# Performance work log

Measured on AMD Instinct MI355X. Metric: run time of the kernel, lower is better.

## Reference

```python
import jax, jax.numpy as jnp
import numpy as np

NUM_HEADS, NUM_KV, HEAD_DIM, WIDTH = 4, 1, 256, 1024
MASK_FILL = -2.3819763e38


def _apply_rope(x, positions, max_wavelength=10000.0):
    # x: [B, T, N, H], positions: [B, T]
    d = x.shape[-1]
    freq_exp = (2.0 / d) * jnp.arange(d // 2, dtype=jnp.float32)
    timescale = max_wavelength ** freq_exp                      # [H/2]
    radians = positions[..., None].astype(jnp.float32) / timescale  # [B, T, H/2]
    radians = radians[..., None, :]                             # [B, T, 1, H/2]
    sin, cos = jnp.sin(radians), jnp.cos(radians)
    x1, x2 = jnp.split(x, 2, axis=-1)
    out = jnp.concatenate([x1 * cos - x2 * sin, x2 * cos + x1 * sin], axis=-1)
    return out.astype(x.dtype)


def _rmsnorm(x, scale):
    var = jnp.mean(jnp.square(x.astype(jnp.float32)), axis=-1, keepdims=True)
    normed = x * jax.lax.rsqrt(var + 1e-6)
    return (normed * (1 + scale)).astype(x.dtype)


def setup_inputs() -> dict:
    key = jax.random.key(0)
    ks = jax.random.split(key, 7)
    B, T, S = 8, 512, 2048
    return {
        "x": jax.random.normal(ks[0], (B, T, WIDTH), jnp.float32),
        "mem_seq": jax.random.normal(ks[1], (B, S, WIDTH), jnp.float32),
        "mem_mask": jax.random.randint(ks[2], (B, S), 0, 2).astype(bool),
        "rms_scale": jax.random.normal(ks[3], (WIDTH,), jnp.float32) * 0.02,
        "q_w": jax.random.normal(ks[4], (NUM_HEADS, WIDTH, HEAD_DIM), jnp.float32) / np.sqrt(WIDTH),
        "kv_w": jax.random.normal(ks[5], (2, NUM_KV, WIDTH, HEAD_DIM), jnp.float32) / np.sqrt(WIDTH),
        "out_w": jax.random.normal(ks[6], (NUM_HEADS, HEAD_DIM, WIDTH), jnp.float32) / np.sqrt(NUM_HEADS * HEAD_DIM),
    }


def reference(x, mem_seq, mem_mask, rms_scale, q_w, kv_w, out_w):
    B, S, _ = mem_seq.shape
    T = x.shape[1]
    G = NUM_HEADS // NUM_KV  # query heads per kv head

    xn = _rmsnorm(x, rms_scale)          # shared RMSNorm params
    mn = _rmsnorm(mem_seq, rms_scale)

    q = jnp.einsum("BTD,NDH->BTNH", xn, q_w)          # [B,T,4,256]
    kv = jnp.einsum("BSD,cKDH->cBSKH", mn, kv_w)      # [2,B,S,1,256]
    k, v = kv[0], kv[1]

    q_pos = jnp.broadcast_to(jnp.arange(S, T + S), (B, T))
    k_pos = jnp.broadcast_to(jnp.arange(S), (B, S))
    q = _apply_rope(q, q_pos) * (HEAD_DIM ** -0.5)
    k = _apply_rope(k, k_pos)

    q = q.reshape(B, T, NUM_KV, G, HEAD_DIM)
    logits = jnp.einsum("BTKGH,BSKH->BKGTS", q, k, preferred_element_type=jnp.float32)
    masked = jnp.where(mem_mask[:, None, None, None, :], logits, MASK_FILL)
    probs = jax.nn.softmax(masked, axis=-1).astype(x.dtype)
    enc = jnp.einsum("BKGTS,BSKH->BTKGH", probs, v).reshape(B, T, NUM_HEADS, HEAD_DIM)
    return jnp.einsum("BTNH,NHD->BTD", enc, out_w)
```

## Files before the change

kernel.cpp:

```cpp
#include <hip/hip_runtime.h>
#include <stdint.h>

typedef __bf16   bf16x8 __attribute__((ext_vector_type(8)));
typedef float    f32x4  __attribute__((ext_vector_type(4)));
typedef float    f32x16 __attribute__((ext_vector_type(16)));
typedef uint16_t u16x8  __attribute__((ext_vector_type(8)));
typedef uint16_t u16x4  __attribute__((ext_vector_type(4)));
typedef uint32_t u32x4  __attribute__((ext_vector_type(4)));

#define DEVFN static __device__ __forceinline__

DEVFN uint16_t f2bf(float f){
  uint32_t u = __builtin_bit_cast(uint32_t, f);
  u += 0x7fffu + ((u >> 16) & 1u);
  return (uint16_t)(u >> 16);
}
DEVFN float bf2f(uint16_t h){
  return __builtin_bit_cast(float, (uint32_t)h << 16);
}
DEVFN bf16x8 ldbf8(const uint16_t* p){
  return __builtin_bit_cast(bf16x8, *(const u16x8*)p);
}
DEVFN void gl16(const void* g, void* l){
  __builtin_amdgcn_global_load_lds((__attribute__((address_space(1))) void*)g,
                                   (__attribute__((address_space(3))) void*)l,
                                   16, 0, 0);
}
DEVFN f32x4 mfma16(bf16x8 a, bf16x8 b, f32x4 c){
  return __builtin_amdgcn_mfma_f32_16x16x32_bf16(a, b, c, 0, 0, 0);
}
DEVFN f32x16 mfma32(bf16x8 a, bf16x8 b, f32x16 c){
  return __builtin_amdgcn_mfma_f32_32x32x16_bf16(a, b, c, 0, 0, 0);
}
DEVFN uint32_t cvtpk(float lo, float hi){
  uint32_t r;
  asm("v_cvt_pk_bf16_f32 %0, %1, %2" : "=v"(r) : "v"(lo), "v"(hi));
  return r;
}
DEVFN void plswap(uint32_t &x, uint32_t &y){
  asm("v_permlane32_swap_b32 %0, %1" : "+v"(x), "+v"(y));
}
DEVFN int permcol(int j){
  return (((j & 127) >> 4) << 5) + (((j >> 7) & 1) << 4) + (j & 15);
}
DEVFN void fastsc(float rad, float& sn, float& cs){
  float rev = rad * 0.15915494309189535f;
  rev = __builtin_amdgcn_fractf(rev);
  sn = __builtin_amdgcn_sinf(rev);
  cs = __builtin_amdgcn_cosf(rev);
}

__global__ void detect_mask_k(const uint32_t* m, int* flag){
  int i = blockIdx.x * 256 + threadIdx.x;
  uint32_t v = m[i];
  int notint   = (v > 1u) ? 1 : 0;
  int notfloat = (v != 0u && v != 0x3F800000u) ? 2 : 0;
  int bits = notint | notfloat;
  if (__any(bits)){
    int agg = bits;
    agg |= __shfl_xor(agg, 1);  agg |= __shfl_xor(agg, 2);
    agg |= __shfl_xor(agg, 4);  agg |= __shfl_xor(agg, 8);
    agg |= __shfl_xor(agg, 16); agg |= __shfl_xor(agg, 32);
    if ((threadIdx.x & 63) == 0) atomicOr(flag, agg);
  }
}

__global__ void expand_mask_k(const void* m, const int* flag, float* bias){
  int i = blockIdx.x * 256 + threadIdx.x;
  int f = *flag;
  bool on;
  if ((f & 1) == 0)      on = ((const int*)m)[i]   != 0;
  else if ((f & 2) == 0) on = ((const float*)m)[i] != 0.0f;
  else                   on = ((const uint8_t*)m)[i] != 0;
  bias[i] = on ? 0.0f : -1e30f;
}

__global__ __launch_bounds__(256) void fused_pre_k(const float* __restrict__ x,
                                                   const float* __restrict__ mem,
                                                   uint16_t* __restrict__ xn,
                                                   uint16_t* __restrict__ mn,
                                                   const float* __restrict__ scale,
                                                   const float* __restrict__ qw,
                                                   const float* __restrict__ kvw,
                                                   const float* __restrict__ ow,
                                                   uint16_t* __restrict__ wq,
                                                   uint16_t* __restrict__ wkv,
                                                   uint16_t* __restrict__ wout){
  int bid = blockIdx.x;
  if (bid < 20480){
    int row = bid;
    const float* in; uint16_t* out; int r0;
    if (row < 4096){ in = x;  out = xn; r0 = row; }
    else           { in = mem; out = mn; r0 = row - 4096; }
    const float4* ip = (const float4*)(in + (size_t)r0 * 1024);
    float4 v = ip[threadIdx.x];
    float ss = v.x*v.x + v.y*v.y + v.z*v.z + v.w*v.w;
    #pragma unroll
    for (int off = 1; off < 64; off <<= 1) ss += __shfl_xor(ss, off);
    __shared__ float wsum[4];
    if ((threadIdx.x & 63) == 0) wsum[threadIdx.x >> 6] = ss;
    __syncthreads();
    float r = rsqrtf((wsum[0] + wsum[1] + wsum[2] + wsum[3]) * (1.0f/1024.0f) + 1e-6f);
    float4 sc = ((const float4*)scale)[threadIdx.x];
    u16x4 o;
    o[0] = f2bf(v.x * r * (1.0f + sc.x));
    o[1] = f2bf(v.y * r * (1.0f + sc.y));
    o[2] = f2bf(v.z * r * (1.0f + sc.z));
    o[3] = f2bf(v.w * r * (1.0f + sc.w));
    *(u16x4*)(out + (size_t)r0 * 1024 + threadIdx.x * 4) = o;
  } else {
    int t = bid - 20480;
    int z = t >> 10, rem = t & 1023;
    int r0 = (rem >> 5) * 32, c0 = (rem & 31) * 32;
    const float* in; uint16_t* out; int rs, C;
    bool perm;
    if (z < 4)      { in = qw  + z*262144;     out = wq  + z*262144;     rs = 256;  C = 256;  perm = true;  }
    else if (z < 6) { in = kvw + (z-4)*262144; out = wkv + (z-4)*262144; rs = 256;  C = 256;  perm = (z == 4); }
    else            { in = ow;                 out = wout;               rs = 1024; C = 1024; perm = false; }
    if (c0 >= C) return;
    __shared__ float tt[32][33];
    int tx = threadIdx.x & 31, ty = threadIdx.x >> 5;
    #pragma unroll
    for (int i = 0; i < 4; ++i)
      tt[ty + 8*i][tx] = in[(size_t)(r0 + ty + 8*i) * rs + c0 + tx];
    __syncthreads();
    #pragma unroll
    for (int i = 0; i < 4; ++i){
      int c = c0 + ty + 8*i;
      int pc = perm ? permcol(c) : c;
      out[(size_t)pc * 1024 + r0 + tx] = f2bf(tt[tx][ty + 8*i]);
    }
  }
}

#define GEMM_BODY(A_, Bt_, K_)                                                  \
  __shared__ __align__(16) uint16_t As[128*64];                                 \
  __shared__ __align__(16) uint16_t Bs[128*64];                                 \
  f32x4 acc[4][4] = {};                                                         \
  {                                                                             \
    const int K = (K_);                                                         \
    _Pragma("unroll 1")                                                         \
    for (int k0 = 0; k0 < K; k0 += 64){                                         \
      __syncthreads();                                                          \
      _Pragma("unroll")                                                         \
      for (int it = 0; it < 4; ++it){                                           \
        int ob = it * 4096 + tid * 16;                                          \
        int row = ob >> 7;                                                      \
        int col = (ob & 127) ^ ((row & 7) << 4);                                \
        gl16((const char*)(A_)  + ((size_t)(m0 + row) * K + k0) * 2 + col,      \
             (char*)As + it * 4096 + wid * 1024);                               \
        gl16((const char*)(Bt_) + ((size_t)(n0 + row) * K + k0) * 2 + col,      \
             (char*)Bs + it * 4096 + wid * 1024);                               \
      }                                                                         \
      __syncthreads();                                                          \
      bf16x8 af[2][4], bfr[2][4];                                               \
      _Pragma("unroll")                                                         \
      for (int ks = 0; ks < 2; ++ks){                                           \
        _Pragma("unroll")                                                       \
        for (int m = 0; m < 4; ++m)                                             \
          af[ks][m]  = ldbf8(&As[(wr*64 + m*16 + lr) * 64 +                     \
                                 ((ks*32 + lq*8) ^ ((lr & 7) << 3))]);          \
        _Pragma("unroll")                                                       \
        for (int n = 0; n < 4; ++n)                                             \
          bfr[ks][n] = ldbf8(&Bs[(wc*64 + n*16 + lr) * 64 +                     \
                                 ((ks*32 + lq*8) ^ ((lr & 7) << 3))]);          \
      }                                                                         \
      _Pragma("unroll")                                                         \
      for (int ks = 0; ks < 2; ++ks)                                            \
        _Pragma("unroll")                                                       \
        for (int m = 0; m < 4; ++m)                                             \
          _Pragma("unroll")                                                     \
          for (int n = 0; n < 4; ++n)                                           \
            acc[m][n] = mfma16(af[ks][m], bfr[ks][n], acc[m][n]);               \
    }                                                                           \
  }

__global__ __launch_bounds__(256) void gemm_qkv_k(const uint16_t* __restrict__ xn,
                                                  const uint16_t* __restrict__ mn,
                                                  const uint16_t* __restrict__ wq,
                                                  const uint16_t* __restrict__ wkv,
                                                  uint16_t* __restrict__ qb,
                                                  uint16_t* __restrict__ kb,
                                                  uint16_t* __restrict__ vt3){
  int bx = blockIdx.x;
  bool isq = bx < 256;
  const uint16_t *A, *Bt;
  int n0, m0;
  if (isq){
    int m = (bx & 7) + 8 * (bx >> 6);
    int n = (bx >> 3) & 7;
    A = xn; Bt = wq;  n0 = n * 128;  m0 = m * 128;
  } else {
    int b2 = bx - 256;
    int m = (b2 & 7) + 8 * (b2 >> 5);
    int n = (b2 >> 3) & 3;
    A = mn; Bt = wkv; n0 = n * 128; m0 = m * 128;
  }
  int tid = threadIdx.x, lane = tid & 63, wid = tid >> 6;
  int wr = wid >> 1, wc = wid & 1;
  int lr = lane & 15, lq = lane >> 4;
  GEMM_BODY(A, Bt, 1024)
  if (isq){
    #pragma unroll
    for (int m = 0; m < 4; ++m){
      int gr0 = m0 + wr*64 + m*16 + lq*4;
      #pragma unroll
      for (int np = 0; np < 2; ++np){
        int gcl = n0 + wc*64 + (2*np)*16 + lr;
        int j = (((gcl & 255) >> 5) << 4) + (gcl & 15);
        float inv = exp2f((float)j * (-13.287712379549449f / 128.0f));
        #pragma unroll
        for (int r = 0; r < 4; ++r){
          float rad = (float)(2048 + ((gr0 + r) & 511)) * inv;
          float sn, cs; fastsc(rad, sn, cs);
          float x1 = acc[m][2*np][r], x2 = acc[m][2*np + 1][r];
          qb[(size_t)(gr0 + r) * 1024 + gcl]      = f2bf((x1*cs - x2*sn) * 0.0625f);
          qb[(size_t)(gr0 + r) * 1024 + gcl + 16] = f2bf((x2*cs + x1*sn) * 0.0625f);
        }
      }
    }
  } else if (n0 < 256){
    #pragma unroll
    for (int m = 0; m < 4; ++m){
      int gr0 = m0 + wr*64 + m*16 + lq*4;
      #pragma unroll
      for (int np = 0; np < 2; ++np){
        int gcl = n0 + wc*64 + (2*np)*16 + lr;
        int j = ((gcl >> 5) << 4) + (gcl & 15);
        float inv = exp2f((float)j * (-13.287712379549449f / 128.0f));
        #pragma unroll
        for (int r = 0; r < 4; ++r){
          float rad = (float)((gr0 + r) & 2047) * inv;
          float sn, cs; fastsc(rad, sn, cs);
          float x1 = acc[m][2*np][r], x2 = acc[m][2*np + 1][r];
          kb[(size_t)(gr0 + r) * 256 + gcl]      = f2bf(x1*cs - x2*sn);
          kb[(size_t)(gr0 + r) * 256 + gcl + 16] = f2bf(x2*cs + x1*sn);
        }
      }
    }
  } else {
    #pragma unroll
    for (int m = 0; m < 4; ++m)
      #pragma unroll
      for (int n = 0; n < 4; ++n){
        int gr0 = m0 + wr*64 + m*16 + lq*4;
        int gc  = n0 + wc*64 + n*16 + lr;
        int h = gc - 256, bb = gr0 >> 11, s0 = gr0 & 2047;
        int st = s0 >> 5, sc = (s0 >> 3) & 3, s8 = s0 & 7;
        u16x4 pk;
        #pragma unroll
        for (int r = 0; r < 4; ++r) pk[r] = f2bf(acc[m][n][r]);
        *(u16x4*)&vt3[((((size_t)bb*64 + st)*4 + sc)*256 + h)*8 + s8] = pk;
      }
  }
}

__global__ __launch_bounds__(256) void gemm_out_k(const uint16_t* __restrict__ A,
                                                  const uint16_t* __restrict__ Bt,
                                                  float* __restrict__ Cf){
  int bx = blockIdx.x;
  int m = (bx & 7) + 8 * (bx >> 6);
  int n = (bx >> 3) & 7;
  int n0 = n * 128, m0 = m * 128;
  int tid = threadIdx.x, lane = tid & 63, wid = tid >> 6;
  int wr = wid >> 1, wc = wid & 1;
  int lr = lane & 15, lq = lane >> 4;
  GEMM_BODY(A, Bt, 1024)
  #pragma unroll
  for (int mm = 0; mm < 4; ++mm)
    #pragma unroll
    for (int nn = 0; nn < 4; ++nn){
      int gr0 = m0 + wr*64 + mm*16 + lq*4;
      int gc  = n0 + wc*64 + nn*16 + lr;
      #pragma unroll
      for (int r = 0; r < 4; ++r) Cf[(size_t)(gr0 + r) * 1024 + gc] = acc[mm][nn][r];
    }
}

__global__ __launch_bounds__(512, 2) void attn_k(const uint16_t* __restrict__ Q,
                                                 const uint16_t* __restrict__ Kb,
                                                 const uint16_t* __restrict__ Vt3,
                                                 const float* __restrict__ bias,
                                                 uint16_t* __restrict__ po,
                                                 uint16_t* __restrict__ po3,
                                                 float* __restrict__ pm,
                                                 float* __restrict__ pl){
  int bx = blockIdx.x;
  int b = bx & 7, qt = (bx >> 3) & 7, sh = bx >> 6;
  int tid = threadIdx.x, lane = tid & 63, wid = tid >> 6;
  int n = wid & 3, qs = wid >> 2;
  int lc = lane & 31, hi = lane >> 5;
  __shared__ __align__(16) uint16_t Ks[3*32*256];
  __shared__ __align__(16) uint16_t Vs[3*4*256*8];
  __shared__ uint32_t mask_lds[16];

  int sbeg = sh * 512;
  {
    float bv = bias[b*2048 + sbeg + tid];
    unsigned long long bal = __ballot(bv == 0.0f);
    if (lane == 0){
      mask_lds[wid*2]     = (uint32_t)bal;
      mask_lds[wid*2 + 1] = (uint32_t)(bal >> 32);
    }
  }

  int t0w = qt*64 + qs*32;
  bf16x8 qf[16];
  {
    const uint16_t* qp = Q + (size_t)(b*512 + t0w + lc) * 1024 + n*256 + hi*8;
    #pragma unroll
    for (int kc = 0; kc < 16; ++kc) qf[kc] = ldbf8(qp + kc*16);
  }
  f32x16 o[8] = {};
  float mrow = -1e30f, lrow = 0.0f;

  auto STAGE = [&](int buf, int s0){
    const char* vsrc = (const char*)Vt3 + ((size_t)(b*64 + (s0 >> 5))) * 16384;
    #pragma unroll
    for (int it = 0; it < 2; ++it){
      int ob = it*8192 + tid*16;
      int krow = ob >> 9;
      int kcol = (ob & 511) ^ ((krow & 7) << 4);
      gl16((const char*)Kb + ((size_t)(b*2048 + s0 + krow) * 256) * 2 + kcol,
           (char*)Ks + buf*16384 + it*8192 + wid*1024);
      gl16(vsrc + ob,
           (char*)Vs + buf*16384 + it*8192 + wid*1024);
    }
  };

  STAGE(0, sbeg);
  STAGE(1, sbeg + 32);

  #pragma unroll 1
  for (int t = 0; t < 16; ++t){
    if (t == 0)      asm volatile("s_waitcnt vmcnt(4) lgkmcnt(0)" ::: "memory");
    else if (t < 15) asm volatile("s_waitcnt vmcnt(4)" ::: "memory");
    else             asm volatile("s_waitcnt vmcnt(0)" ::: "memory");
    __builtin_amdgcn_s_barrier();
    asm volatile("" ::: "memory");
    if (t < 14) STAGE((t+2)%3, sbeg + (t+2)*32);

    const uint16_t* ksb = Ks + (t%3)*8192;
    const uint16_t* vsb = Vs + (t%3)*8192;

    f32x16 sacc = {};
    __builtin_amdgcn_s_setprio(1);
    #pragma unroll
    for (int kc = 0; kc < 16; ++kc){
      bf16x8 ak = ldbf8(&ksb[lc*256 + ((kc*16 + hi*8) ^ ((lc & 7) << 3))]);
      sacc = mfma32(ak, qf[kc], sacc);
    }
    __builtin_amdgcn_s_setprio(0);

    uint32_t mw = mask_lds[t];
    int sb4 = hi * 4;
    float p[16];
    float mx = -1e30f;
    #pragma unroll
    for (int r = 0; r < 16; ++r){
      int sr = (r & 3) + 8*(r >> 2) + sb4;
      float v = ((mw >> sr) & 1u) ? sacc[r] : -1e30f;
      p[r] = v;
      mx = fmaxf(mx, v);
    }
    mx = fmaxf(mx, __shfl_xor(mx, 32));
    if (__any(mx > mrow + 8.0f)){
      float mn = fmaxf(mrow, mx);
      float scl = __expf(mrow - mn);
      mrow = mn; lrow *= scl;
      #pragma unroll
      for (int ht = 0; ht < 8; ++ht) o[ht] *= scl;
    }
    float rs = 0.0f;
    #pragma unroll
    for (int r = 0; r < 16; ++r){ p[r] = __expf(p[r] - mrow); rs += p[r]; }
    rs += __shfl_xor(rs, 32);
    lrow += rs;

    uint32_t w0, w1, w2, w3, w4, w5, w6, w7;
    w0 = cvtpk(p[0], p[1]);   w2 = cvtpk(p[4], p[5]);   plswap(w0, w2);
    w1 = cvtpk(p[2], p[3]);   w3 = cvtpk(p[6], p[7]);   plswap(w1, w3);
    w4 = cvtpk(p[8], p[9]);   w6 = cvtpk(p[12], p[13]); plswap(w4, w6);
    w5 = cvtpk(p[10], p[11]); w7 = cvtpk(p[14], p[15]); plswap(w5, w7);
    u32x4 t0v = {w0, w1, w2, w3};
    u32x4 t1v = {w4, w5, w6, w7};
    bf16x8 pa0 = __builtin_bit_cast(bf16x8, t0v);
    bf16x8 pa1 = __builtin_bit_cast(bf16x8, t1v);

    __builtin_amdgcn_s_setprio(1);
    #pragma unroll
    for (int ht = 0; ht < 8; ++ht){
      bf16x8 bv0 = ldbf8(&vsb[(size_t)hi*2048       + (ht*32 + lc)*8]);
      o[ht] = mfma32(pa0, bv0, o[ht]);
      bf16x8 bv1 = ldbf8(&vsb[(size_t)(2 + hi)*2048 + (ht*32 + lc)*8]);
      o[ht] = mfma32(pa1, bv1, o[ht]);
    }
    __builtin_amdgcn_s_setprio(0);
  }

  uint16_t* pop = (sh == 3) ? po3 : po + (size_t)sh * 4194304;
  #pragma unroll
  for (int ht = 0; ht < 8; ++ht)
    #pragma unroll
    for (int r = 0; r < 16; ++r){
      int qr = (r & 3) + 8*(r >> 2) + hi*4;
      pop[(size_t)(b*512 + t0w + qr)*1024 + n*256 + ht*32 + lc] = f2bf(o[ht][r]);
    }
  if (hi == 0){
    int mlidx = sh*16384 + (b*512 + t0w + lc)*4 + n;
    pm[mlidx] = mrow;
    pl[mlidx] = lrow;
  }
}

__global__ __launch_bounds__(64) void merge_k(const uint16_t* __restrict__ po,
                                              const uint16_t* __restrict__ po3,
                                              const float* __restrict__ pm,
                                              const float* __restrict__ pl,
                                              uint16_t* __restrict__ enc){
  int idx = blockIdx.x;
  int row = idx >> 2, n = idx & 3;
  float m = -1e30f;
  #pragma unroll
  for (int h = 0; h < 4; ++h) m = fmaxf(m, pm[h*16384 + idx]);
  float w[4], lsum = 0.0f;
  #pragma unroll
  for (int h = 0; h < 4; ++h){
    w[h] = __expf(pm[h*16384 + idx] - m);
    lsum += pl[h*16384 + idx] * w[h];
  }
  float inv = 1.0f / lsum;
  size_t off = (size_t)row*1024 + n*256 + threadIdx.x*4;
  float acc[4] = {0.f, 0.f, 0.f, 0.f};
  #pragma unroll
  for (int h = 0; h < 4; ++h){
    const uint16_t* src = (h < 3) ? po + (size_t)h*4194304 + off : po3 + off;
    u16x4 a = *(const u16x4*)src;
    #pragma unroll
    for (int r = 0; r < 4; ++r) acc[r] += bf2f(a[r]) * w[h];
  }
  u16x4 ov;
  #pragma unroll
  for (int r = 0; r < 4; ++r) ov[r] = f2bf(acc[r] * inv);
  *(u16x4*)(enc + off) = ov;
}

extern "C" void kernel_launch(void* const* d_in, const int* in_sizes, int n_in,
                              void* d_out, int out_size, void* d_ws, size_t ws_size,
                              hipStream_t stream){
  const float* x    = (const float*)d_in[0];
  const float* mem  = (const float*)d_in[1];
  const void*  mask = d_in[2];
  const float* rms  = (const float*)d_in[3];
  const float* qw   = (const float*)d_in[4];
  const float* kvw  = (const float*)d_in[5];
  const float* ow   = (const float*)d_in[6];
  float* out = (float*)d_out;
  char* ws = (char*)d_ws;

  uint16_t* xn   = (uint16_t*)(ws + 0);
  uint16_t* enc  = (uint16_t*)(ws + 0);
  const size_t MB = 1ull << 20;
  uint16_t* qb   = (uint16_t*)(ws + 8*MB);
  uint16_t* kb   = (uint16_t*)(ws + 16*MB);
  uint16_t* vt3  = (uint16_t*)(ws + 24*MB);
  uint16_t* wq   = (uint16_t*)(ws + 32*MB);
  float*    pm   = (float*)   (ws + 32*MB);
  float*    pl   = (float*)   (ws + 32*MB + 262144);
  uint16_t* wkv  = (uint16_t*)(ws + 34*MB);
  uint16_t* wout = (uint16_t*)(ws + 35*MB);
  float*    bias = (float*)   (ws + 37*MB);
  int*      flag = (int*)     (ws + 37*MB + 65536);
  uint16_t* mn   = (uint16_t*)(ws + 38*MB);
  uint16_t* po   = (uint16_t*)(ws + 38*MB);
  uint16_t* po3  = (uint16_t*)out;

  hipMemsetAsync(flag, 0, 4, stream);
  detect_mask_k<<<16, 256, 0, stream>>>((const uint32_t*)mask, flag);
  expand_mask_k<<<64, 256, 0, stream>>>(mask, flag, bias);

  fused_pre_k<<<27648, 256, 0, stream>>>(x, mem, xn, mn, rms, qw, kvw, ow, wq, wkv, wout);

  gemm_qkv_k<<<768, 256, 0, stream>>>(xn, mn, wq, wkv, qb, kb, vt3);

  attn_k<<<256, 512, 0, stream>>>(qb, kb, vt3, bias, po, po3, pm, pl);
  merge_k<<<16384, 64, 0, stream>>>(po, po3, pm, pl, enc);

  gemm_out_k<<<256, 256, 0, stream>>>(enc, wout, out);
}
```

Before: 163.1 us.

## Triple-buffer GEMM K-tiles with async global-to-LDS prefetch

Rewrites the shared GEMM body into a three-stage pipeline with K-tiles of 32. Tiles t+1 and t+2 are loaded into LDS while tile t is computed, using a vmcnt wait and a single barrier per step in place of two syncthreads. The aim is to hide global load latency behind the MFMA work. The XOR swizzle is dropped, so the 64-byte LDS rows may cause bank conflicts, and the smaller tile doubles the number of loop iterations and barriers.

```diff
diff --git a/kernel.cpp b/kernel.cpp
--- a/kernel.cpp
+++ b/kernel.cpp
@@ -134,44 +134,46 @@
 }
 
 #define GEMM_BODY(A_, Bt_, K_)                                                  \
-  __shared__ __align__(16) uint16_t As[128*64];                                 \
-  __shared__ __align__(16) uint16_t Bs[128*64];                                 \
+  __shared__ __align__(16) uint16_t As[3*128*32];                               \
+  __shared__ __align__(16) uint16_t Bs[3*128*32];                               \
   f32x4 acc[4][4] = {};                                                         \
   {                                                                             \
     const int K = (K_);                                                         \
+    const int NT = K / 32;                                                      \
+    auto STAGEG = [&](int buf, int k0){                                         \
+      _Pragma("unroll")                                                         \
+      for (int it = 0; it < 2; ++it){                                           \
+        int ob = it * 4096 + tid * 16;                                          \
+        int row = ob >> 6, col = ob & 63;                                       \
+        gl16((const char*)(A_)  + ((size_t)(m0 + row) * K + k0) * 2 + col,      \
+             (char*)As + buf * 8192 + it * 4096 + wid * 1024);                  \
+        gl16((const char*)(Bt_) + ((size_t)(n0 + row) * K + k0) * 2 + col,      \
+             (char*)Bs + buf * 8192 + it * 4096 + wid * 1024);                  \
+      }                                                                         \
+    };                                                                          \
+    STAGEG(0, 0);                                                               \
+    STAGEG(1, 32);                                                              \
     _Pragma("unroll 1")                                                         \
-    for (int k0 = 0; k0 < K; k0 += 64){                                         \
-      __syncthreads();                                                          \
+    for (int t = 0; t < NT; ++t){                                               \
+      if (t < NT - 1) asm volatile("s_waitcnt vmcnt(4)" ::: "memory");          \
+      else            asm volatile("s_waitcnt vmcnt(0)" ::: "memory");          \
+      __builtin_amdgcn_s_barrier();                                             \
+      asm volatile("" ::: "memory");                                            \
+      if (t < NT - 2) STAGEG((t + 2) % 3, (t + 2) * 32);                        \
+      const uint16_t* as = As + (t % 3) * 4096;                                 \
+      const uint16_t* bs = Bs + (t % 3) * 4096;                                 \
+      bf16x8 af[4], bfr[4];                                                     \
       _Pragma("unroll")                                                         \
-      for (int it = 0; it < 4; ++it){                                           \
-        int ob = it * 4096 + tid * 16;                                          \
-        int row = ob >> 7;                                                      \
-        int col = (ob & 127) ^ ((row & 7) << 4);                                \
-        gl16((const char*)(A_)  + ((size_t)(m0 + row) * K + k0) * 2 + col,      \
-             (char*)As + it * 4096 + wid * 1024);                               \
-        gl16((const char*)(Bt_) + ((size_t)(n0 + row) * K + k0) * 2 + col,      \
-             (char*)Bs + it * 4096 + wid * 1024);                               \
-      }                                                                         \
-      __syncthreads();                                                          \
-      bf16x8 af[2][4], bfr[2][4];                                               \
+      for (int m = 0; m < 4; ++m)                                               \
+        af[m]  = ldbf8(&as[(wr*64 + m*16 + lr) * 32 + lq * 8]);                 \
       _Pragma("unroll")                                                         \
-      for (int ks = 0; ks < 2; ++ks){                                           \
-        _Pragma("unroll")                                                       \
-        for (int m = 0; m < 4; ++m)                                             \
-          af[ks][m]  = ldbf8(&As[(wr*64 + m*16 + lr) * 64 +                     \
-                                 ((ks*32 + lq*8) ^ ((lr & 7) << 3))]);          \
+      for (int n = 0; n < 4; ++n)                                               \
+        bfr[n] = ldbf8(&bs[(wc*64 + n*16 + lr) * 32 + lq * 8]);                 \
+      _Pragma("unroll")                                                         \
+      for (int m = 0; m < 4; ++m)                                               \
         _Pragma("unroll")                                                       \
         for (int n = 0; n < 4; ++n)                                             \
-          bfr[ks][n] = ldbf8(&Bs[(wc*64 + n*16 + lr) * 64 +                     \
-                                 ((ks*32 + lq*8) ^ ((lr & 7) << 3))]);          \
-      }                                                                         \
-      _Pragma("unroll")                                                         \
-      for (int ks = 0; ks < 2; ++ks)                                            \
-        _Pragma("unroll")                                                       \
-        for (int m = 0; m < 4; ++m)                                             \
-          _Pragma("unroll")                                                     \
-          for (int n = 0; n < 4; ++n)                                           \
-            acc[m][n] = mfma16(af[ks][m], bfr[ks][n], acc[m][n]);               \
+          acc[m][n] = mfma16(af[m], bfr[n], acc[m][n]);                         \
     }                                                                           \
   }
 
```

After: 169.7 us. +4.0%, slower.
